# Optimization experiments

Measured on AMD Instinct MI355X. Metric: run time of the kernel, lower is better.

Reference implementation:

```python
import jax, jax.numpy as jnp
import numpy as np

N = 100_000      # total nodes across batch of graphs
E = 1_600_000    # total directed edges
D = 128          # input feature dim
H = 128          # hidden dim
OUT = 10         # output classes
B = 500          # number of graphs (200 nodes each)
L_MID = 3        # GIN layers after the first (num_layers-2)


def setup_inputs() -> dict:
    key = jax.random.key(0)
    ks = jax.random.split(key, 24)
    s = np.float32(1.0 / np.sqrt(H))
    f32 = jnp.float32
    inp = {
        'node_features': jax.random.normal(ks[0], (N, D), f32),
        'edge_src': jax.random.randint(ks[1], (E,), 0, N, jnp.int32),
        'edge_dst': jax.random.randint(ks[2], (E,), 0, N, jnp.int32),
        'graph_ids': (jnp.arange(N) // (N // B)).astype(jnp.int32),
        # GIN eps per layer (torch init: zeros)
        'eps': jnp.zeros((4,), f32),
        # pre MLP (input layer): Linear(D,H) -> BN -> ReLU -> Linear(H,H), then pre_batchnorm
        'pre_W1': jax.random.normal(ks[3], (D, H), f32) * s,
        'pre_b1': jnp.zeros((H,), f32),
        'pre_g1': jnp.ones((H,), f32),
        'pre_bt1': jnp.zeros((H,), f32),
        'pre_W2': jax.random.normal(ks[4], (H, H), f32) * s,
        'pre_b2': jnp.zeros((H,), f32),
        'pre_gout': jnp.ones((H,), f32),
        'pre_btout': jnp.zeros((H,), f32),
        # middle GIN layers (stacked over L_MID)
        'mlp_W1': jax.random.normal(ks[5], (L_MID, H, H), f32) * s,
        'mlp_b1': jnp.zeros((L_MID, H), f32),
        'mlp_g1': jnp.ones((L_MID, H), f32),
        'mlp_bt1': jnp.zeros((L_MID, H), f32),
        'mlp_W2': jax.random.normal(ks[6], (L_MID, H, H), f32) * s,
        'mlp_b2': jnp.zeros((L_MID, H), f32),
        'bn_g': jnp.ones((L_MID, H), f32),
        'bn_bt': jnp.zeros((L_MID, H), f32),
        # per-layer prediction heads
        'pred_W0': jax.random.normal(ks[7], (D, OUT), f32) * s,
        'pred_b0': jnp.zeros((OUT,), f32),
        'pred_W': jax.random.normal(ks[8], (4, H, OUT), f32) * s,
        'pred_b': jnp.zeros((4, OUT), f32),
    }
    return inp


def _mlp_bn(x, W1, b1, g1, bt1, W2, b2, go, bo):
    # MLP(num_mlp_layers=2): Linear -> BN(eval) -> ReLU -> Linear, then outer BN(eval) -> ReLU
    h = jax.nn.relu(g1 * (x @ W1 + b1) + bt1)
    h = h @ W2 + b2
    return jax.nn.relu(go * h + bo)


def reference(node_features, edge_src, edge_dst, graph_ids, eps,
              pre_W1, pre_b1, pre_g1, pre_bt1, pre_W2, pre_b2, pre_gout, pre_btout,
              mlp_W1, mlp_b1, mlp_g1, mlp_bt1, mlp_W2, mlp_b2, bn_g, bn_bt,
              pred_W0, pred_b0, pred_W, pred_b):
    def agg(h):
        # sparse Adj @ h via gather + segment_sum (sum neighbor pooling, learn_eps=True -> no self loops)
        return jax.ops.segment_sum(h[edge_src], edge_dst, num_segments=N)

    h = node_features
    reps = [h]
    pooled = agg(h) + (1.0 + eps[0]) * h
    h = _mlp_bn(pooled, pre_W1, pre_b1, pre_g1, pre_bt1, pre_W2, pre_b2, pre_gout, pre_btout)
    reps.append(h)
    for i in range(L_MID):
        pooled = agg(h) + (1.0 + eps[i + 1]) * h
        h = _mlp_bn(pooled, mlp_W1[i], mlp_b1[i], mlp_g1[i], mlp_bt1[i],
                    mlp_W2[i], mlp_b2[i], bn_g[i], bn_bt[i])
        reps.append(h)

    # graph-level sum pooling + per-layer linear heads (dropout off in eval)
    score = jax.ops.segment_sum(reps[0], graph_ids, num_segments=B) @ pred_W0 + pred_b0
    for k in range(4):
        score = score + jax.ops.segment_sum(reps[k + 1], graph_ids, num_segments=B) @ pred_W[k] + pred_b[k]
    return score  # [B, OUT]
```

## Files before the change

kernel.cpp:

```cpp
#include <hip/hip_runtime.h>
#include <hip/hip_bf16.h>

#define NN 100000
#define EE 1600000
#define HH 128
#define OUTC 10
#define BB 500
#define GSZ 200
#define LDA 136

#define NBKT 782
#define BCAP 2560
#define EPB 4096
#define NBUCKB 391
#define NTILE64 1563

typedef float f32x4 __attribute__((ext_vector_type(4)));
typedef __bf16 bf16x8 __attribute__((ext_vector_type(8)));

__device__ __forceinline__ float b2f(unsigned short u){
    unsigned int x = ((unsigned int)u) << 16;
    return __builtin_bit_cast(float, x);
}
__device__ __forceinline__ unsigned short f2b(float f){
    __hip_bfloat16 h = __float2bfloat16(f);
    return __builtin_bit_cast(unsigned short, h);
}

__global__ __launch_bounds__(256) void k_setup(const int* __restrict__ src, const int* __restrict__ dst,
                                               int* __restrict__ bucket_cursor, unsigned int* __restrict__ ebuf,
                                               const float* __restrict__ x, unsigned short* __restrict__ hA,
                                               float* __restrict__ G,
                                               const float* __restrict__ preW1, const float* __restrict__ preW2,
                                               const float* __restrict__ mlpW1, const float* __restrict__ mlpW2,
                                               unsigned short* __restrict__ Wbf){
    __shared__ __align__(16) unsigned int sval[EPB];
    __shared__ unsigned short sbkt[EPB];
    __shared__ int shist[NBKT];
    int t = threadIdx.x;
    int bid = blockIdx.x;

    if (bid < NBUCKB){
        int e0 = bid * EPB;
        for (int i = t; i < NBKT; i += 256) shist[i] = 0;
        __syncthreads();
        for (int i = t; i < EPB; i += 256){
            int e = e0 + i;
            if (e < EE){
                int d = dst[e];
                int b = d >> 7;
                sval[i] = ((unsigned)src[e] << 7) | (unsigned)(d & 127);
                sbkt[i] = (unsigned short)b;
                atomicAdd(&shist[b], 1);
            } else {
                sbkt[i] = 0xffff;
            }
        }
        __syncthreads();
        for (int i = t; i < NBKT; i += 256){
            int c = shist[i];
            shist[i] = c ? atomicAdd(&bucket_cursor[i], c) : 0;
        }
        __syncthreads();
        for (int i = t; i < EPB; i += 256){
            unsigned short b = sbkt[i];
            if (b != 0xffff){
                int pos = atomicAdd(&shist[b], 1);
                if (pos < BCAP) ebuf[(int)b * BCAP + pos] = sval[i];
            }
        }
    } else if (bid < NBUCKB + BB){
        float* r0 = (float*)sval;
        float* r1 = r0 + 256;
        int g = bid - NBUCKB;
        int f2 = t & 63;
        int rg = t >> 6;
        if (t < 128){
            #pragma unroll
            for (int k = 1; k < 5; ++k) G[(size_t)k*BB*128 + g*128 + t] = 0.f;
        }
        float a0 = 0.f, a1 = 0.f;
        for (int i = rg; i < GSZ; i += 4){
            int node = g*GSZ + i;
            float2 v = *(const float2*)(x + (size_t)node*128 + f2*2);
            a0 += v.x; a1 += v.y;
            unsigned int o = (unsigned)f2b(v.x) | ((unsigned)f2b(v.y) << 16);
            ((unsigned int*)hA)[(size_t)node*64 + f2] = o;
        }
        r0[t] = a0; r1[t] = a1;
        __syncthreads();
        if (t < 64){
            float s0 = r0[t] + r0[t+64] + r0[t+128] + r0[t+192];
            float s1 = r1[t] + r1[t+64] + r1[t+128] + r1[t+192];
            float2 v; v.x = s0; v.y = s1;
            *(float2*)(G + g*128 + t*2) = v;
        }
    } else {
        int idx = (bid - NBUCKB - BB)*256 + t;
        int w = idx >> 14;
        int rem = idx & 16383;
        int e = rem & 7;
        int chunk = rem >> 3;
        int m = chunk & 15;
        int q = (chunk >> 4) & 3;
        int kk = (chunk >> 6) & 3;
        int j = chunk >> 8;
        int n = j*16 + m;
        int k = kk*32 + q*8 + e;
        const float* s;
        if      (w == 0) s = preW1;
        else if (w == 1) s = preW2;
        else if (w <  5) s = mlpW1 + (w-2)*16384;
        else             s = mlpW2 + (w-5)*16384;
        Wbf[idx] = f2b(s[k*128 + n]);
    }
}

__global__ __launch_bounds__(1024) void k_bscan(const int* __restrict__ bucket_cursor,
                                                int* __restrict__ bucket_base, int* __restrict__ row_ptr){
    __shared__ int tmp[1024];
    int t = threadIdx.x;
    int v = (t < NBKT) ? min(bucket_cursor[t], BCAP) : 0;
    tmp[t] = v; __syncthreads();
    for (int off = 1; off < 1024; off <<= 1){
        int a = (t >= off) ? tmp[t - off] : 0;
        __syncthreads();
        tmp[t] += a;
        __syncthreads();
    }
    if (t < NBKT) bucket_base[t + 1] = tmp[t];
    if (t == 0){ bucket_base[0] = 0; row_ptr[NN] = EE; }
}

__global__ __launch_bounds__(256) void k_csr(const int* __restrict__ bucket_cursor, const int* __restrict__ bucket_base,
                                             const unsigned int* __restrict__ ebuf,
                                             int* __restrict__ row_ptr, int* __restrict__ col){
    __shared__ int cnt[128];
    __shared__ int pfx[128];
    int b = blockIdx.x;
    int t = threadIdx.x;
    int c    = min(bucket_cursor[b], BCAP);
    int base = bucket_base[b];
    if (t < 128) cnt[t] = 0;
    __syncthreads();
    const unsigned int* eb = ebuf + (size_t)b * BCAP;
    for (int i = t; i < c; i += 256) atomicAdd(&cnt[eb[i] & 127], 1);
    __syncthreads();
    if (t == 0){
        int run = 0;
        for (int i = 0; i < 128; ++i){ pfx[i] = run; run += cnt[i]; }
    }
    __syncthreads();
    int node0 = b * 128;
    if (t < 128 && node0 + t < NN) row_ptr[node0 + t] = base + pfx[t];
    if (t < 128) cnt[t] = pfx[t];
    __syncthreads();
    for (int i = t; i < c; i += 256){
        unsigned int v = eb[i];
        int pos = atomicAdd(&cnt[v & 127], 1);
        col[base + pos] = (int)(v >> 7);
    }
}

__device__ __forceinline__ void acc_u32(float* a, unsigned int v, int j){
    a[j]   += __builtin_bit_cast(float, v << 16);
    a[j+1] += __builtin_bit_cast(float, v & 0xffff0000u);
}
__device__ __forceinline__ void acc_u4(float* a, uint4 v){
    acc_u32(a, v.x, 0); acc_u32(a, v.y, 2); acc_u32(a, v.z, 4); acc_u32(a, v.w, 6);
}
__device__ __forceinline__ uint4 and4(uint4 v, unsigned mk){
    v.x &= mk; v.y &= mk; v.z &= mk; v.w &= mk; return v;
}

__global__ __launch_bounds__(256) void k_agg(const int* __restrict__ row_ptr, const int* __restrict__ col,
                                             const unsigned short* __restrict__ h,
                                             const float* __restrict__ eps, int l,
                                             unsigned short* __restrict__ pooled){
    int lane = threadIdx.x & 63;
    int wv   = threadIdx.x >> 6;
    int n    = blockIdx.x*4 + wv;
    int q = lane >> 4;
    int u = lane & 15;
    int beg = row_ptr[n], end = row_ptr[n+1];
    float a[8];
    #pragma unroll
    for (int j = 0; j < 8; ++j) a[j] = 0.f;

    int e = beg;
    for (; e + 16 <= end; e += 16){
        int c0 = col[e      + q];
        int c1 = col[e + 4  + q];
        int c2 = col[e + 8  + q];
        int c3 = col[e + 12 + q];
        uint4 v0 = *(const uint4*)(h + (size_t)c0*128 + u*8);
        uint4 v1 = *(const uint4*)(h + (size_t)c1*128 + u*8);
        uint4 v2 = *(const uint4*)(h + (size_t)c2*128 + u*8);
        uint4 v3 = *(const uint4*)(h + (size_t)c3*128 + u*8);
        acc_u4(a, v0); acc_u4(a, v1); acc_u4(a, v2); acc_u4(a, v3);
    }
    if (e < end){
        int last = end - 1;
        int i0 = e + q, i1 = e + 4 + q, i2 = e + 8 + q, i3 = e + 12 + q;
        int c0 = col[min(i0, last)];
        int c1 = col[min(i1, last)];
        int c2 = col[min(i2, last)];
        int c3 = col[min(i3, last)];
        uint4 v0 = *(const uint4*)(h + (size_t)c0*128 + u*8);
        uint4 v1 = *(const uint4*)(h + (size_t)c1*128 + u*8);
        uint4 v2 = *(const uint4*)(h + (size_t)c2*128 + u*8);
        uint4 v3 = *(const uint4*)(h + (size_t)c3*128 + u*8);
        v0 = and4(v0, (i0 < end) ? 0xffffffffu : 0u);
        v1 = and4(v1, (i1 < end) ? 0xffffffffu : 0u);
        v2 = and4(v2, (i2 < end) ? 0xffffffffu : 0u);
        v3 = and4(v3, (i3 < end) ? 0xffffffffu : 0u);
        acc_u4(a, v0); acc_u4(a, v1); acc_u4(a, v2); acc_u4(a, v3);
    }
    #pragma unroll
    for (int j = 0; j < 8; ++j){
        a[j] += __shfl_xor(a[j], 16, 64);
        a[j] += __shfl_xor(a[j], 32, 64);
    }
    if (q == 0){
        float ep = 1.0f + eps[l];
        uint4 hs = *(const uint4*)(h + (size_t)n*128 + u*8);
        a[0] += ep * __builtin_bit_cast(float, hs.x << 16);
        a[1] += ep * __builtin_bit_cast(float, hs.x & 0xffff0000u);
        a[2] += ep * __builtin_bit_cast(float, hs.y << 16);
        a[3] += ep * __builtin_bit_cast(float, hs.y & 0xffff0000u);
        a[4] += ep * __builtin_bit_cast(float, hs.z << 16);
        a[5] += ep * __builtin_bit_cast(float, hs.z & 0xffff0000u);
        a[6] += ep * __builtin_bit_cast(float, hs.w << 16);
        a[7] += ep * __builtin_bit_cast(float, hs.w & 0xffff0000u);
        uint4 o;
        o.x = (unsigned)f2b(a[0]) | ((unsigned)f2b(a[1]) << 16);
        o.y = (unsigned)f2b(a[2]) | ((unsigned)f2b(a[3]) << 16);
        o.z = (unsigned)f2b(a[4]) | ((unsigned)f2b(a[5]) << 16);
        o.w = (unsigned)f2b(a[6]) | ((unsigned)f2b(a[7]) << 16);
        *(uint4*)(pooled + (size_t)n*128 + u*8) = o;
    }
}

__device__ __forceinline__ void load_a(const unsigned short* __restrict__ Ain, int tile,
                                       int wv, int m, int q, bf16x8* dst){
    int node = tile*64 + wv*16 + m;
    bool valid = node < NN;
    const unsigned short* base = Ain + (size_t)(valid ? node : 0)*128 + q*8;
    #pragma unroll
    for (int kk = 0; kk < 4; ++kk){
        int4 v = *(const int4*)(base + kk*32);
        if (!valid) v = make_int4(0,0,0,0);
        dst[kk] = __builtin_bit_cast(bf16x8, v);
    }
}

__global__ __launch_bounds__(256, 4) void k_mlp1(const unsigned short* __restrict__ Ain,
                                                 unsigned short* __restrict__ Yout,
                                                 const unsigned short* __restrict__ Wf,
                                                 const float* __restrict__ bb, const float* __restrict__ gg,
                                                 const float* __restrict__ bt){
    __shared__ __align__(16) unsigned short Wl[16384];
    __shared__ __align__(16) unsigned short Ys[4][16*LDA];
    int t = threadIdx.x;
    int lane = t & 63, wv = t >> 6;
    int m = lane & 15, q = lane >> 4;
    for (int i = t; i < 2048; i += 256)
        *(int4*)(&Wl[i*8]) = *(const int4*)(Wf + i*8);
    __syncthreads();
    float ge[8], ce[8];
    #pragma unroll
    for (int j = 0; j < 8; ++j){
        int colc = j*16 + m;
        float gv = gg[colc];
        ge[j] = gv; ce[j] = bb[colc]*gv + bt[colc];
    }
    unsigned short* Y = &Ys[wv][0];
    int tile = blockIdx.x;
    bf16x8 aN[4];
    if (tile < NTILE64) load_a(Ain, tile, wv, m, q, aN);
    while (tile < NTILE64){
        bf16x8 a[4];
        #pragma unroll
        for (int kk = 0; kk < 4; ++kk) a[kk] = aN[kk];
        int nxt = tile + gridDim.x;
        if (nxt < NTILE64) load_a(Ain, nxt, wv, m, q, aN);
        f32x4 acc[8];
        #pragma unroll
        for (int j = 0; j < 8; ++j) acc[j] = (f32x4){0.f,0.f,0.f,0.f};
        #pragma unroll
        for (int kk = 0; kk < 4; ++kk){
            #pragma unroll
            for (int j = 0; j < 8; ++j){
                bf16x8 b = *(const bf16x8*)(&Wl[((((j*4+kk)*4+q)*16)+m)*8]);
                acc[j] = __builtin_amdgcn_mfma_f32_16x16x32_bf16(a[kk], b, acc[j], 0, 0, 0);
            }
        }
        #pragma unroll
        for (int j = 0; j < 8; ++j){
            int colc = j*16 + m;
            #pragma unroll
            for (int r = 0; r < 4; ++r){
                float v = fmaxf(acc[j][r]*ge[j] + ce[j], 0.f);
                Y[(q*4 + r)*LDA + colc] = f2b(v);
            }
        }
        #pragma unroll
        for (int i = 0; i < 4; ++i){
            int idx = i*64 + lane;
            int r = idx >> 4, c = idx & 15;
            int nd = tile*64 + wv*16 + r;
            if (nd < NN)
                *(int4*)(Yout + (size_t)nd*128 + c*8) = *(const int4*)(&Y[r*LDA + c*8]);
        }
        tile = nxt;
    }
}

__global__ __launch_bounds__(256, 4) void k_mlp2(const unsigned short* __restrict__ Ain,
                                                 unsigned short* __restrict__ Out,
                                                 const unsigned short* __restrict__ Wf,
                                                 const float* __restrict__ bb, const float* __restrict__ gg,
                                                 const float* __restrict__ bt,
                                                 float* __restrict__ Gout){
    __shared__ __align__(16) unsigned short Wl[16384];
    __shared__ __align__(16) unsigned short Ys[4][16*LDA];
    int t = threadIdx.x;
    int lane = t & 63, wv = t >> 6;
    int m = lane & 15, q = lane >> 4;
    for (int i = t; i < 2048; i += 256)
        *(int4*)(&Wl[i*8]) = *(const int4*)(Wf + i*8);
    __syncthreads();
    float ge[8], ce[8];
    #pragma unroll
    for (int j = 0; j < 8; ++j){
        int colc = j*16 + m;
        float gv = gg[colc];
        ge[j] = gv; ce[j] = bb[colc]*gv + bt[colc];
    }
    unsigned short* Y = &Ys[wv][0];
    int tile = blockIdx.x;
    bf16x8 aN[4];
    if (tile < NTILE64) load_a(Ain, tile, wv, m, q, aN);
    while (tile < NTILE64){
        bf16x8 a[4];
        #pragma unroll
        for (int kk = 0; kk < 4; ++kk) a[kk] = aN[kk];
        int nxt = tile + gridDim.x;
        if (nxt < NTILE64) load_a(Ain, nxt, wv, m, q, aN);
        f32x4 acc[8];
        #pragma unroll
        for (int j = 0; j < 8; ++j) acc[j] = (f32x4){0.f,0.f,0.f,0.f};
        #pragma unroll
        for (int kk = 0; kk < 4; ++kk){
            #pragma unroll
            for (int j = 0; j < 8; ++j){
                bf16x8 b = *(const bf16x8*)(&Wl[((((j*4+kk)*4+q)*16)+m)*8]);
                acc[j] = __builtin_amdgcn_mfma_f32_16x16x32_bf16(a[kk], b, acc[j], 0, 0, 0);
            }
        }
        #pragma unroll
        for (int j = 0; j < 8; ++j){
            int colc = j*16 + m;
            #pragma unroll
            for (int r = 0; r < 4; ++r){
                float v = fmaxf(acc[j][r]*ge[j] + ce[j], 0.f);
                Y[(q*4 + r)*LDA + colc] = f2b(v);
            }
        }
        int row0 = tile*64 + wv*16;
        #pragma unroll
        for (int i = 0; i < 4; ++i){
            int idx = i*64 + lane;
            int r = idx >> 4, c = idx & 15;
            int nd = row0 + r;
            if (nd < NN)
                *(int4*)(Out + (size_t)nd*128 + c*8) = *(const int4*)(&Y[r*LDA + c*8]);
        }
        {
            float run0 = 0.f, run1 = 0.f;
            int curg = row0 / GSZ;
            for (int r = 0; r < 16; ++r){
                int nd = row0 + r;
                if (nd >= NN) break;
                int g = nd / GSZ;
                if (g != curg){
                    if (run0 != 0.f) atomicAdd(&Gout[curg*128 + lane*2], run0);
                    if (run1 != 0.f) atomicAdd(&Gout[curg*128 + lane*2 + 1], run1);
                    run0 = 0.f; run1 = 0.f; curg = g;
                }
                unsigned int v = *(const unsigned int*)(&Y[r*LDA + lane*2]);
                run0 += b2f((unsigned short)v);
                run1 += b2f((unsigned short)(v >> 16));
            }
            if (run0 != 0.f) atomicAdd(&Gout[curg*128 + lane*2], run0);
            if (run1 != 0.f) atomicAdd(&Gout[curg*128 + lane*2 + 1], run1);
        }
        tile = nxt;
    }
}

__global__ __launch_bounds__(256) void k_score(const float* __restrict__ G,
                                               const float* __restrict__ W0, const float* __restrict__ b0,
                                               const float* __restrict__ Wk, const float* __restrict__ bk,
                                               float* __restrict__ out){
    int id = blockIdx.x*256 + threadIdx.x;
    if (id >= BB*OUTC) return;
    int b = id / OUTC, o = id % OUTC;
    float s = b0[o];
    #pragma unroll
    for (int k = 0; k < 4; ++k) s += bk[k*OUTC + o];
    const float* g0 = G + b*128;
    for (int c = 0; c < 128; ++c) s += g0[c] * W0[c*OUTC + o];
    for (int k = 0; k < 4; ++k){
        const float* gk = G + (size_t)(k+1)*BB*128 + b*128;
        const float* wk = Wk + k*128*OUTC;
        for (int c = 0; c < 128; ++c) s += gk[c] * wk[c*OUTC + o];
    }
    out[id] = s;
}

extern "C" void kernel_launch(void* const* d_in, const int* in_sizes, int n_in,
                              void* d_out, int out_size, void* d_ws, size_t ws_size,
                              hipStream_t stream){
    const float* node_features = (const float*)d_in[0];
    const int*   edge_src  = (const int*)d_in[1];
    const int*   edge_dst  = (const int*)d_in[2];
    const float* eps       = (const float*)d_in[4];
    const float* pre_W1    = (const float*)d_in[5];
    const float* pre_b1    = (const float*)d_in[6];
    const float* pre_g1    = (const float*)d_in[7];
    const float* pre_bt1   = (const float*)d_in[8];
    const float* pre_W2    = (const float*)d_in[9];
    const float* pre_b2    = (const float*)d_in[10];
    const float* pre_gout  = (const float*)d_in[11];
    const float* pre_btout = (const float*)d_in[12];
    const float* mlp_W1    = (const float*)d_in[13];
    const float* mlp_b1    = (const float*)d_in[14];
    const float* mlp_g1    = (const float*)d_in[15];
    const float* mlp_bt1   = (const float*)d_in[16];
    const float* mlp_W2    = (const float*)d_in[17];
    const float* mlp_b2    = (const float*)d_in[18];
    const float* bn_g      = (const float*)d_in[19];
    const float* bn_bt     = (const float*)d_in[20];
    const float* pred_W0   = (const float*)d_in[21];
    const float* pred_b0   = (const float*)d_in[22];
    const float* pred_W    = (const float*)d_in[23];
    const float* pred_b    = (const float*)d_in[24];
    float* out = (float*)d_out;

    char* p = (char*)d_ws;
    auto alloc = [&](size_t bytes)->char*{
        char* r = p;
        p += (bytes + 255) & ~(size_t)255;
        return r;
    };
    int* bucket_cursor    = (int*)alloc((size_t)NBKT*4);
    int* bucket_base      = (int*)alloc((size_t)(NBKT+1)*4);
    int* row_ptr          = (int*)alloc((size_t)(NN+1)*4);
    int* col              = (int*)alloc((size_t)EE*4);
    unsigned int* ebuf    = (unsigned int*)alloc((size_t)NBKT*BCAP*4);
    unsigned short* Wbf   = (unsigned short*)alloc((size_t)8*128*128*2);
    unsigned short* hA    = (unsigned short*)alloc((size_t)NN*128*2);
    unsigned short* hB    = (unsigned short*)alloc((size_t)NN*128*2);
    unsigned short* pooled= (unsigned short*)alloc((size_t)NN*128*2);
    float* G              = (float*)alloc((size_t)5*BB*128*4);

    hipMemsetAsync(bucket_cursor, 0, (size_t)NBKT*4, stream);

    k_setup<<<NBUCKB + BB + 512, 256, 0, stream>>>(edge_src, edge_dst, bucket_cursor, ebuf,
                                                   node_features, hA, G,
                                                   pre_W1, pre_W2, mlp_W1, mlp_W2, Wbf);
    k_bscan<<<1, 1024, 0, stream>>>(bucket_cursor, bucket_base, row_ptr);
    k_csr<<<NBKT, 256, 0, stream>>>(bucket_cursor, bucket_base, ebuf, row_ptr, col);

    const unsigned short* hcur = hA;
    unsigned short* hnxt = hB;
    for (int l = 0; l < 4; ++l){
        k_agg<<<NN/4, 256, 0, stream>>>(row_ptr, col, hcur, eps, l, pooled);
        const unsigned short *W1t, *W2t;
        const float *b1,*g1,*bt1,*b2,*g2,*bt2;
        if (l == 0){
            W1t = Wbf;             W2t = Wbf + 16384;
            b1 = pre_b1; g1 = pre_g1; bt1 = pre_bt1;
            b2 = pre_b2; g2 = pre_gout; bt2 = pre_btout;
        } else {
            W1t = Wbf + (size_t)(2 + (l-1))*16384;
            W2t = Wbf + (size_t)(5 + (l-1))*16384;
            b1 = mlp_b1 + (l-1)*128; g1 = mlp_g1 + (l-1)*128; bt1 = mlp_bt1 + (l-1)*128;
            b2 = mlp_b2 + (l-1)*128; g2 = bn_g   + (l-1)*128; bt2 = bn_bt   + (l-1)*128;
        }
        k_mlp1<<<768, 256, 0, stream>>>(pooled, pooled, W1t, b1, g1, bt1);
        k_mlp2<<<768, 256, 0, stream>>>(pooled, hnxt, W2t, b2, g2, bt2,
                                        G + (size_t)(l+1)*BB*128);
        const unsigned short* tmp = hnxt;
        hnxt = (unsigned short*)hcur;
        hcur = tmp;
    }
    k_score<<<(BB*OUTC + 255)/256, 256, 0, stream>>>(G, pred_W0, pred_b0, pred_W, pred_b, out);
}
```

Before: 609.3 us.

## Assign one node per quarter-wave in aggregation and widen MLP blocks to 512 threads

```diff
diff --git a/kernel.cpp b/kernel.cpp
--- a/kernel.cpp
+++ b/kernel.cpp
@@ -13,7 +13,7 @@
 #define BCAP 2560
 #define EPB 4096
 #define NBUCKB 391
-#define NTILE64 1563
+#define NTILE128 782
 
 typedef float f32x4 __attribute__((ext_vector_type(4)));
 typedef __bf16 bf16x8 __attribute__((ext_vector_type(8)));
@@ -169,9 +169,6 @@
 __device__ __forceinline__ void acc_u4(float* a, uint4 v){
     acc_u32(a, v.x, 0); acc_u32(a, v.y, 2); acc_u32(a, v.z, 4); acc_u32(a, v.w, 6);
 }
-__device__ __forceinline__ uint4 and4(uint4 v, unsigned mk){
-    v.x &= mk; v.y &= mk; v.z &= mk; v.w &= mk; return v;
-}
 
 __global__ __launch_bounds__(256) void k_agg(const int* __restrict__ row_ptr, const int* __restrict__ col,
                                              const unsigned short* __restrict__ h,
@@ -179,71 +176,49 @@
                                              unsigned short* __restrict__ pooled){
     int lane = threadIdx.x & 63;
     int wv   = threadIdx.x >> 6;
-    int n    = blockIdx.x*4 + wv;
     int q = lane >> 4;
     int u = lane & 15;
+    int n = blockIdx.x*16 + wv*4 + q;
     int beg = row_ptr[n], end = row_ptr[n+1];
     float a[8];
     #pragma unroll
     for (int j = 0; j < 8; ++j) a[j] = 0.f;
 
     int e = beg;
-    for (; e + 16 <= end; e += 16){
-        int c0 = col[e      + q];
-        int c1 = col[e + 4  + q];
-        int c2 = col[e + 8  + q];
-        int c3 = col[e + 12 + q];
+    for (; e + 4 <= end; e += 4){
+        int c0 = col[e], c1 = col[e+1], c2 = col[e+2], c3 = col[e+3];
         uint4 v0 = *(const uint4*)(h + (size_t)c0*128 + u*8);
         uint4 v1 = *(const uint4*)(h + (size_t)c1*128 + u*8);
         uint4 v2 = *(const uint4*)(h + (size_t)c2*128 + u*8);
         uint4 v3 = *(const uint4*)(h + (size_t)c3*128 + u*8);
         acc_u4(a, v0); acc_u4(a, v1); acc_u4(a, v2); acc_u4(a, v3);
     }
-    if (e < end){
-        int last = end - 1;
-        int i0 = e + q, i1 = e + 4 + q, i2 = e + 8 + q, i3 = e + 12 + q;
-        int c0 = col[min(i0, last)];
-        int c1 = col[min(i1, last)];
-        int c2 = col[min(i2, last)];
-        int c3 = col[min(i3, last)];
-        uint4 v0 = *(const uint4*)(h + (size_t)c0*128 + u*8);
-        uint4 v1 = *(const uint4*)(h + (size_t)c1*128 + u*8);
-        uint4 v2 = *(const uint4*)(h + (size_t)c2*128 + u*8);
-        uint4 v3 = *(const uint4*)(h + (size_t)c3*128 + u*8);
-        v0 = and4(v0, (i0 < end) ? 0xffffffffu : 0u);
-        v1 = and4(v1, (i1 < end) ? 0xffffffffu : 0u);
-        v2 = and4(v2, (i2 < end) ? 0xffffffffu : 0u);
-        v3 = and4(v3, (i3 < end) ? 0xffffffffu : 0u);
-        acc_u4(a, v0); acc_u4(a, v1); acc_u4(a, v2); acc_u4(a, v3);
-    }
-    #pragma unroll
-    for (int j = 0; j < 8; ++j){
-        a[j] += __shfl_xor(a[j], 16, 64);
-        a[j] += __shfl_xor(a[j], 32, 64);
-    }
-    if (q == 0){
-        float ep = 1.0f + eps[l];
-        uint4 hs = *(const uint4*)(h + (size_t)n*128 + u*8);
-        a[0] += ep * __builtin_bit_cast(float, hs.x << 16);
-        a[1] += ep * __builtin_bit_cast(float, hs.x & 0xffff0000u);
-        a[2] += ep * __builtin_bit_cast(float, hs.y << 16);
-        a[3] += ep * __builtin_bit_cast(float, hs.y & 0xffff0000u);
-        a[4] += ep * __builtin_bit_cast(float, hs.z << 16);
-        a[5] += ep * __builtin_bit_cast(float, hs.z & 0xffff0000u);
-        a[6] += ep * __builtin_bit_cast(float, hs.w << 16);
-        a[7] += ep * __builtin_bit_cast(float, hs.w & 0xffff0000u);
-        uint4 o;
-        o.x = (unsigned)f2b(a[0]) | ((unsigned)f2b(a[1]) << 16);
-        o.y = (unsigned)f2b(a[2]) | ((unsigned)f2b(a[3]) << 16);
-        o.z = (unsigned)f2b(a[4]) | ((unsigned)f2b(a[5]) << 16);
-        o.w = (unsigned)f2b(a[6]) | ((unsigned)f2b(a[7]) << 16);
-        *(uint4*)(pooled + (size_t)n*128 + u*8) = o;
-    }
-}
-
-__device__ __forceinline__ void load_a(const unsigned short* __restrict__ Ain, int tile,
-                                       int wv, int m, int q, bf16x8* dst){
-    int node = tile*64 + wv*16 + m;
+    for (; e < end; ++e){
+        int c = col[e];
+        uint4 v = *(const uint4*)(h + (size_t)c*128 + u*8);
+        acc_u4(a, v);
+    }
+    float ep = 1.0f + eps[l];
+    uint4 hs = *(const uint4*)(h + (size_t)n*128 + u*8);
+    a[0] += ep * __builtin_bit_cast(float, hs.x << 16);
+    a[1] += ep * __builtin_bit_cast(float, hs.x & 0xffff0000u);
+    a[2] += ep * __builtin_bit_cast(float, hs.y << 16);
+    a[3] += ep * __builtin_bit_cast(float, hs.y & 0xffff0000u);
+    a[4] += ep * __builtin_bit_cast(float, hs.z << 16);
+    a[5] += ep * __builtin_bit_cast(float, hs.z & 0xffff0000u);
+    a[6] += ep * __builtin_bit_cast(float, hs.w << 16);
+    a[7] += ep * __builtin_bit_cast(float, hs.w & 0xffff0000u);
+    uint4 o;
+    o.x = (unsigned)f2b(a[0]) | ((unsigned)f2b(a[1]) << 16);
+    o.y = (unsigned)f2b(a[2]) | ((unsigned)f2b(a[3]) << 16);
+    o.z = (unsigned)f2b(a[4]) | ((unsigned)f2b(a[5]) << 16);
+    o.w = (unsigned)f2b(a[6]) | ((unsigned)f2b(a[7]) << 16);
+    *(uint4*)(pooled + (size_t)n*128 + u*8) = o;
+}
+
+__device__ __forceinline__ void load_a(const unsigned short* __restrict__ Ain, int row0,
+                                       int m, int q, bf16x8* dst){
+    int node = row0 + m;
     bool valid = node < NN;
     const unsigned short* base = Ain + (size_t)(valid ? node : 0)*128 + q*8;
     #pragma unroll
@@ -254,17 +229,17 @@
     }
 }
 
-__global__ __launch_bounds__(256, 4) void k_mlp1(const unsigned short* __restrict__ Ain,
+__global__ __launch_bounds__(512, 4) void k_mlp1(const unsigned short* __restrict__ Ain,
                                                  unsigned short* __restrict__ Yout,
                                                  const unsigned short* __restrict__ Wf,
                                                  const float* __restrict__ bb, const float* __restrict__ gg,
                                                  const float* __restrict__ bt){
     __shared__ __align__(16) unsigned short Wl[16384];
-    __shared__ __align__(16) unsigned short Ys[4][16*LDA];
+    __shared__ __align__(16) unsigned short Ys[8][16*LDA];
     int t = threadIdx.x;
     int lane = t & 63, wv = t >> 6;
     int m = lane & 15, q = lane >> 4;
-    for (int i = t; i < 2048; i += 256)
+    for (int i = t; i < 2048; i += 512)
         *(int4*)(&Wl[i*8]) = *(const int4*)(Wf + i*8);
     __syncthreads();
     float ge[8], ce[8];
@@ -277,13 +252,14 @@
     unsigned short* Y = &Ys[wv][0];
     int tile = blockIdx.x;
     bf16x8 aN[4];
-    if (tile < NTILE64) load_a(Ain, tile, wv, m, q, aN);
-    while (tile < NTILE64){
+    if (tile < NTILE128) load_a(Ain, tile*128 + wv*16, m, q, aN);
+    while (tile < NTILE128){
+        int row0 = tile*128 + wv*16;
         bf16x8 a[4];
         #pragma unroll
         for (int kk = 0; kk < 4; ++kk) a[kk] = aN[kk];
         int nxt = tile + gridDim.x;
-        if (nxt < NTILE64) load_a(Ain, nxt, wv, m, q, aN);
+        if (nxt < NTILE128) load_a(Ain, nxt*128 + wv*16, m, q, aN);
         f32x4 acc[8];
         #pragma unroll
         for (int j = 0; j < 8; ++j) acc[j] = (f32x4){0.f,0.f,0.f,0.f};
@@ -308,7 +284,7 @@
         for (int i = 0; i < 4; ++i){
             int idx = i*64 + lane;
             int r = idx >> 4, c = idx & 15;
-            int nd = tile*64 + wv*16 + r;
+            int nd = row0 + r;
             if (nd < NN)
                 *(int4*)(Yout + (size_t)nd*128 + c*8) = *(const int4*)(&Y[r*LDA + c*8]);
         }
@@ -316,18 +292,18 @@
     }
 }
 
-__global__ __launch_bounds__(256, 4) void k_mlp2(const unsigned short* __restrict__ Ain,
+__global__ __launch_bounds__(512, 4) void k_mlp2(const unsigned short* __restrict__ Ain,
                                                  unsigned short* __restrict__ Out,
                                                  const unsigned short* __restrict__ Wf,
                                                  const float* __restrict__ bb, const float* __restrict__ gg,
                                                  const float* __restrict__ bt,
                                                  float* __restrict__ Gout){
     __shared__ __align__(16) unsigned short Wl[16384];
-    __shared__ __align__(16) unsigned short Ys[4][16*LDA];
+    __shared__ __align__(16) unsigned short Ys[8][16*LDA];
     int t = threadIdx.x;
     int lane = t & 63, wv = t >> 6;
     int m = lane & 15, q = lane >> 4;
-    for (int i = t; i < 2048; i += 256)
+    for (int i = t; i < 2048; i += 512)
         *(int4*)(&Wl[i*8]) = *(const int4*)(Wf + i*8);
     __syncthreads();
     float ge[8], ce[8];
@@ -340,13 +316,14 @@
     unsigned short* Y = &Ys[wv][0];
     int tile = blockIdx.x;
     bf16x8 aN[4];
-    if (tile < NTILE64) load_a(Ain, tile, wv, m, q, aN);
-    while (tile < NTILE64){
+    if (tile < NTILE128) load_a(Ain, tile*128 + wv*16, m, q, aN);
+    while (tile < NTILE128){
+        int row0 = tile*128 + wv*16;
         bf16x8 a[4];
         #pragma unroll
         for (int kk = 0; kk < 4; ++kk) a[kk] = aN[kk];
         int nxt = tile + gridDim.x;
-        if (nxt < NTILE64) load_a(Ain, nxt, wv, m, q, aN);
+        if (nxt < NTILE128) load_a(Ain, nxt*128 + wv*16, m, q, aN);
         f32x4 acc[8];
         #pragma unroll
         for (int j = 0; j < 8; ++j) acc[j] = (f32x4){0.f,0.f,0.f,0.f};
@@ -367,7 +344,6 @@
                 Y[(q*4 + r)*LDA + colc] = f2b(v);
             }
         }
-        int row0 = tile*64 + wv*16;
         #pragma unroll
         for (int i = 0; i < 4; ++i){
             int idx = i*64 + lane;
@@ -476,7 +452,7 @@
     const unsigned short* hcur = hA;
     unsigned short* hnxt = hB;
     for (int l = 0; l < 4; ++l){
-        k_agg<<<NN/4, 256, 0, stream>>>(row_ptr, col, hcur, eps, l, pooled);
+        k_agg<<<NN/16, 256, 0, stream>>>(row_ptr, col, hcur, eps, l, pooled);
         const unsigned short *W1t, *W2t;
         const float *b1,*g1,*bt1,*b2,*g2,*bt2;
         if (l == 0){
@@ -489,8 +465,8 @@
             b1 = mlp_b1 + (l-1)*128; g1 = mlp_g1 + (l-1)*128; bt1 = mlp_bt1 + (l-1)*128;
             b2 = mlp_b2 + (l-1)*128; g2 = bn_g   + (l-1)*128; bt2 = bn_bt   + (l-1)*128;
         }
-        k_mlp1<<<768, 256, 0, stream>>>(pooled, pooled, W1t, b1, g1, bt1);
-        k_mlp2<<<768, 256, 0, stream>>>(pooled, hnxt, W2t, b2, g2, bt2,
+        k_mlp1<<<512, 512, 0, stream>>>(pooled, pooled, W1t, b1, g1, bt1);
+        k_mlp2<<<512, 512, 0, stream>>>(pooled, hnxt, W2t, b2, g2, bt2,
                                         G + (size_t)(l+1)*BB*128);
         const unsigned short* tmp = hnxt;
         hnxt = (unsigned short*)hcur;
```

Measured after the change: 881.2 us. +44.6%, slower.

## Fuse the two MLP linear layers into one kernel, keeping the intermediate in LDS

Applied to the files above, without the earlier changes.

```diff
diff --git a/kernel.cpp b/kernel.cpp
--- a/kernel.cpp
+++ b/kernel.cpp
@@ -241,9 +241,9 @@
     }
 }
 
-__device__ __forceinline__ void load_a(const unsigned short* __restrict__ Ain, int tile,
-                                       int wv, int m, int q, bf16x8* dst){
-    int node = tile*64 + wv*16 + m;
+__device__ __forceinline__ void load_a(const unsigned short* __restrict__ Ain, int row0,
+                                       int m, int q, bf16x8* dst){
+    int node = row0 + m;
     bool valid = node < NN;
     const unsigned short* base = Ain + (size_t)(valid ? node : 0)*128 + q*8;
     #pragma unroll
@@ -254,73 +254,14 @@
     }
 }
 
-__global__ __launch_bounds__(256, 4) void k_mlp1(const unsigned short* __restrict__ Ain,
-                                                 unsigned short* __restrict__ Yout,
-                                                 const unsigned short* __restrict__ Wf,
-                                                 const float* __restrict__ bb, const float* __restrict__ gg,
-                                                 const float* __restrict__ bt){
-    __shared__ __align__(16) unsigned short Wl[16384];
-    __shared__ __align__(16) unsigned short Ys[4][16*LDA];
-    int t = threadIdx.x;
-    int lane = t & 63, wv = t >> 6;
-    int m = lane & 15, q = lane >> 4;
-    for (int i = t; i < 2048; i += 256)
-        *(int4*)(&Wl[i*8]) = *(const int4*)(Wf + i*8);
-    __syncthreads();
-    float ge[8], ce[8];
-    #pragma unroll
-    for (int j = 0; j < 8; ++j){
-        int colc = j*16 + m;
-        float gv = gg[colc];
-        ge[j] = gv; ce[j] = bb[colc]*gv + bt[colc];
-    }
-    unsigned short* Y = &Ys[wv][0];
-    int tile = blockIdx.x;
-    bf16x8 aN[4];
-    if (tile < NTILE64) load_a(Ain, tile, wv, m, q, aN);
-    while (tile < NTILE64){
-        bf16x8 a[4];
-        #pragma unroll
-        for (int kk = 0; kk < 4; ++kk) a[kk] = aN[kk];
-        int nxt = tile + gridDim.x;
-        if (nxt < NTILE64) load_a(Ain, nxt, wv, m, q, aN);
-        f32x4 acc[8];
-        #pragma unroll
-        for (int j = 0; j < 8; ++j) acc[j] = (f32x4){0.f,0.f,0.f,0.f};
-        #pragma unroll
-        for (int kk = 0; kk < 4; ++kk){
-            #pragma unroll
-            for (int j = 0; j < 8; ++j){
-                bf16x8 b = *(const bf16x8*)(&Wl[((((j*4+kk)*4+q)*16)+m)*8]);
-                acc[j] = __builtin_amdgcn_mfma_f32_16x16x32_bf16(a[kk], b, acc[j], 0, 0, 0);
-            }
-        }
-        #pragma unroll
-        for (int j = 0; j < 8; ++j){
-            int colc = j*16 + m;
-            #pragma unroll
-            for (int r = 0; r < 4; ++r){
-                float v = fmaxf(acc[j][r]*ge[j] + ce[j], 0.f);
-                Y[(q*4 + r)*LDA + colc] = f2b(v);
-            }
-        }
-        #pragma unroll
-        for (int i = 0; i < 4; ++i){
-            int idx = i*64 + lane;
-            int r = idx >> 4, c = idx & 15;
-            int nd = tile*64 + wv*16 + r;
-            if (nd < NN)
-                *(int4*)(Yout + (size_t)nd*128 + c*8) = *(const int4*)(&Y[r*LDA + c*8]);
-        }
-        tile = nxt;
-    }
-}
-
-__global__ __launch_bounds__(256, 4) void k_mlp2(const unsigned short* __restrict__ Ain,
+__global__ __launch_bounds__(256, 3) void k_mlpf(const unsigned short* __restrict__ Ain,
                                                  unsigned short* __restrict__ Out,
-                                                 const unsigned short* __restrict__ Wf,
-                                                 const float* __restrict__ bb, const float* __restrict__ gg,
-                                                 const float* __restrict__ bt,
+                                                 const unsigned short* __restrict__ W1f,
+                                                 const unsigned short* __restrict__ W2f,
+                                                 const float* __restrict__ b1, const float* __restrict__ g1,
+                                                 const float* __restrict__ bt1,
+                                                 const float* __restrict__ b2, const float* __restrict__ g2,
+                                                 const float* __restrict__ bt2,
                                                  float* __restrict__ Gout){
     __shared__ __align__(16) unsigned short Wl[16384];
     __shared__ __align__(16) unsigned short Ys[4][16*LDA];
@@ -328,25 +269,28 @@
     int lane = t & 63, wv = t >> 6;
     int m = lane & 15, q = lane >> 4;
     for (int i = t; i < 2048; i += 256)
-        *(int4*)(&Wl[i*8]) = *(const int4*)(Wf + i*8);
+        *(int4*)(&Wl[i*8]) = *(const int4*)(W1f + i*8);
     __syncthreads();
-    float ge[8], ce[8];
+    float ge1[8], ce1[8], ge2[8], ce2[8];
     #pragma unroll
     for (int j = 0; j < 8; ++j){
         int colc = j*16 + m;
-        float gv = gg[colc];
-        ge[j] = gv; ce[j] = bb[colc]*gv + bt[colc];
+        float gv = g1[colc];
+        ge1[j] = gv; ce1[j] = b1[colc]*gv + bt1[colc];
+        gv = g2[colc];
+        ge2[j] = gv; ce2[j] = b2[colc]*gv + bt2[colc];
     }
     unsigned short* Y = &Ys[wv][0];
     int tile = blockIdx.x;
     bf16x8 aN[4];
-    if (tile < NTILE64) load_a(Ain, tile, wv, m, q, aN);
+    if (tile < NTILE64) load_a(Ain, tile*64 + wv*16, m, q, aN);
     while (tile < NTILE64){
+        int row0 = tile*64 + wv*16;
         bf16x8 a[4];
         #pragma unroll
         for (int kk = 0; kk < 4; ++kk) a[kk] = aN[kk];
         int nxt = tile + gridDim.x;
-        if (nxt < NTILE64) load_a(Ain, nxt, wv, m, q, aN);
+        if (nxt < NTILE64) load_a(Ain, nxt*64 + wv*16, m, q, aN);
         f32x4 acc[8];
         #pragma unroll
         for (int j = 0; j < 8; ++j) acc[j] = (f32x4){0.f,0.f,0.f,0.f};
@@ -363,11 +307,32 @@
             int colc = j*16 + m;
             #pragma unroll
             for (int r = 0; r < 4; ++r){
-                float v = fmaxf(acc[j][r]*ge[j] + ce[j], 0.f);
+                float v = fmaxf(acc[j][r]*ge1[j] + ce1[j], 0.f);
                 Y[(q*4 + r)*LDA + colc] = f2b(v);
             }
         }
-        int row0 = tile*64 + wv*16;
+        #pragma unroll
+        for (int kk = 0; kk < 4; ++kk)
+            a[kk] = *(const bf16x8*)(&Y[m*LDA + kk*32 + q*8]);
+        #pragma unroll
+        for (int j = 0; j < 8; ++j) acc[j] = (f32x4){0.f,0.f,0.f,0.f};
+        #pragma unroll
+        for (int kk = 0; kk < 4; ++kk){
+            #pragma unroll
+            for (int j = 0; j < 8; ++j){
+                bf16x8 b = *(const bf16x8*)(W2f + ((((j*4+kk)*4+q)*16)+m)*8);
+                acc[j] = __builtin_amdgcn_mfma_f32_16x16x32_bf16(a[kk], b, acc[j], 0, 0, 0);
+            }
+        }
+        #pragma unroll
+        for (int j = 0; j < 8; ++j){
+            int colc = j*16 + m;
+            #pragma unroll
+            for (int r = 0; r < 4; ++r){
+                float v = fmaxf(acc[j][r]*ge2[j] + ce2[j], 0.f);
+                Y[(q*4 + r)*LDA + colc] = f2b(v);
+            }
+        }
         #pragma unroll
         for (int i = 0; i < 4; ++i){
             int idx = i*64 + lane;
@@ -489,8 +454,7 @@
             b1 = mlp_b1 + (l-1)*128; g1 = mlp_g1 + (l-1)*128; bt1 = mlp_bt1 + (l-1)*128;
             b2 = mlp_b2 + (l-1)*128; g2 = bn_g   + (l-1)*128; bt2 = bn_bt   + (l-1)*128;
         }
-        k_mlp1<<<768, 256, 0, stream>>>(pooled, pooled, W1t, b1, g1, bt1);
-        k_mlp2<<<768, 256, 0, stream>>>(pooled, hnxt, W2t, b2, g2, bt2,
+        k_mlpf<<<768, 256, 0, stream>>>(pooled, hnxt, W1t, W2t, b1,g1,bt1, b2,g2,bt2,
                                         G + (size_t)(l+1)*BB*128);
         const unsigned short* tmp = hnxt;
         hnxt = (unsigned short*)hcur;
```

After: 653.3 us. 7.2% more time.
